# Optimization experiments

Measured on AMD Instinct MI355X. Metric: run time of the kernel, lower is better.

The kernel has to match this reference:

```python
import math
import jax, jax.numpy as jnp
import numpy as np

MODEL_DIM = 256
NUM_HEADS = 8
HEAD_DIM = MODEL_DIM // NUM_HEADS
B, S = 4, 2048


def setup_inputs() -> dict:
    key = jax.random.key(0)
    ks = jax.random.split(key, 9)
    d = MODEL_DIM
    lim = 1.0 / math.sqrt(d)  # torch nn.Linear init range
    def lin(k):
        k1, k2 = jax.random.split(k)
        W = jax.random.uniform(k1, (d, d), jnp.float32, -lim, lim)
        b = jax.random.uniform(k2, (d,), jnp.float32, -lim, lim)
        return W, b
    Wq, bq = lin(ks[0])
    Wk, bk = lin(ks[1])
    Wv, bv = lin(ks[2])
    Wo, bo = lin(ks[3])
    q = jax.random.normal(ks[4], (B, S, d), jnp.float32)
    q_mask = jnp.ones((B, S), dtype=bool)
    return {"q": q, "q_mask": q_mask, "Wq": Wq, "bq": bq, "Wk": Wk, "bk": bk,
            "Wv": Wv, "bv": bv, "Wo": Wo, "bo": bo}


def reference(q, q_mask, Wq, bq, Wk, bk, Wv, bv, Wo, bo):
    b, s, d = q.shape
    h, hd = NUM_HEADS, HEAD_DIM
    # merge_masks: kv_mask defaults to q_mask (self-attention), pad_mask -> float bias
    pad = q_mask[:, :, None] & q_mask[:, None, :]            # [b, s, s] recv x send
    bias = jnp.where(pad, 0.0, -jnp.inf).astype(q.dtype)      # additive attn bias
    # projections, split heads: [b, s, d] -> [b, h, s, hd]
    def proj(x, W, bb):
        return (x @ W.T + bb).reshape(b, s, h, hd).transpose(0, 2, 1, 3)
    qh = proj(q, Wq, bq)
    kh = proj(q, Wk, bk)
    vh = proj(q, Wv, bv)
    # NOTE: original scales by sqrt(model_dim), not sqrt(head_dim)
    qh = qh / math.sqrt(d)
    scores = jnp.einsum('bhqe,bhke->bhqk', qh, kh) + bias[:, None, :, :]
    attn = jax.nn.softmax(scores, axis=-1)
    out = jnp.einsum('bhqk,bhke->bhqe', attn, vh)             # [b, h, s, hd]
    out = out.transpose(0, 2, 1, 3).reshape(b, s, d)
    out = out @ Wo.T + bo
    return jnp.nan_to_num(out)
```

## Files before the change

### kernel.cpp

```cpp
#include <hip/hip_runtime.h>
#include <hip/hip_bf16.h>

typedef __attribute__((ext_vector_type(8))) short bf16x8;
typedef __attribute__((ext_vector_type(4))) short bf16x4;
typedef __attribute__((ext_vector_type(4))) float f32x4;
typedef unsigned short ushort_t;
typedef unsigned int uint_t;

__device__ __forceinline__ ushort_t f2bf(float f) {
  unsigned int u = __builtin_bit_cast(unsigned int, f);
  u += 0x7fffu + ((u >> 16) & 1u);
  return (ushort_t)(u >> 16);
}

__device__ __forceinline__ bf16x8 cvt8(f32x4 a, f32x4 b) {
  bf16x8 r;
  r[0] = (short)f2bf(a[0]); r[1] = (short)f2bf(a[1]);
  r[2] = (short)f2bf(a[2]); r[3] = (short)f2bf(a[3]);
  r[4] = (short)f2bf(b[0]); r[5] = (short)f2bf(b[1]);
  r[6] = (short)f2bf(b[2]); r[7] = (short)f2bf(b[3]);
  return r;
}

#if __has_builtin(__builtin_amdgcn_exp2f)
#define EXP2(x) __builtin_amdgcn_exp2f(x)
#else
#define EXP2(x) __expf(0.69314718056f * (x))
#endif

__device__ __forceinline__ f32x4 mfma16(bf16x4 a, bf16x4 b, f32x4 c) {
#if __has_builtin(__builtin_amdgcn_mfma_f32_16x16x16bf16_1k)
  return __builtin_amdgcn_mfma_f32_16x16x16bf16_1k(a, b, c, 0, 0, 0);
#else
  f32x4 d;
  asm volatile(
      "v_mfma_f32_16x16x16_bf16 %0, %1, %2, %3\n\ts_nop 7\n\ts_nop 7"
      : "=&v"(d)
      : "v"(a), "v"(b), "v"(c));
  return d;
#endif
}

__device__ __forceinline__ void gld_lds16(const void* g, void* l) {
  __builtin_amdgcn_global_load_lds(
      (const __attribute__((address_space(1))) unsigned int*)g,
      (__attribute__((address_space(3))) unsigned int*)l, 16, 0, 0);
}

__global__ __launch_bounds__(256) void prep2_kernel(
    const float* __restrict__ x, const float* __restrict__ Wq,
    const float* __restrict__ Wk, const float* __restrict__ Wv,
    const float* __restrict__ Wo, ushort_t* __restrict__ xb,
    ushort_t* __restrict__ Wb, ushort_t* __restrict__ Wob) {
  const int blk = blockIdx.x;
  const float* src;
  ushort_t* dst;
  int base;
  if (blk < 1024)      { src = x;  dst = xb;          base = blk * 2048; }
  else if (blk < 1056) { src = Wq; dst = Wb;          base = (blk - 1024) * 2048; }
  else if (blk < 1088) { src = Wk; dst = Wb + 65536;  base = (blk - 1056) * 2048; }
  else if (blk < 1120) { src = Wv; dst = Wb + 131072; base = (blk - 1088) * 2048; }
  else                 { src = Wo; dst = Wob;         base = (blk - 1120) * 2048; }
  const int i = base + threadIdx.x * 8;
  const f32x4 a = *(const f32x4*)(src + i);
  const f32x4 b = *(const f32x4*)(src + i + 4);
  *(bf16x8*)(dst + i) = cvt8(a, b);
}

__global__ __launch_bounds__(256) void qkv2_kernel(
    const ushort_t* __restrict__ xb, const ushort_t* __restrict__ Wb,
    const float* __restrict__ bq, const float* __restrict__ bk,
    const float* __restrict__ bv, ushort_t* __restrict__ qh,
    ushort_t* __restrict__ kh, ushort_t* __restrict__ vT) {
  __shared__ ushort_t Xs[2][2][2048], Ws[2][2][2048];
  const int tid = threadIdx.x;
  const int wid = tid >> 6, lane = tid & 63;
  const int l15 = lane & 15, lg = lane >> 4;
  const int row0 = blockIdx.x * 64;
  const int col0 = blockIdx.y * 64;
  const bool isV = (blockIdx.y >= 8);
  const char* XpB = (const char*)(xb + (size_t)row0 * 256);
  const char* WpB = (const char*)(Wb + (size_t)col0 * 256);
  const uint_t gsrc =
      (uint_t)((tid >> 2) * 512 + (((tid & 3) ^ ((tid >> 3) & 3)) << 4));
  const int kswz = (lg ^ ((l15 >> 1) & 3)) << 4;
  const int mrow = (wid >> 1) * 32, ncol = (wid & 1) * 32;
  f32x4 acc[2][2] = {};

#define STG(buf, t)                                                   \
  {                                                                   \
    gld_lds16(XpB + (t) * 64 + gsrc, (char*)Xs[buf][0] + wid * 1024); \
    gld_lds16(XpB + ((t) + 1) * 64 + gsrc,                            \
              (char*)Xs[buf][1] + wid * 1024);                        \
    gld_lds16(WpB + (t) * 64 + gsrc, (char*)Ws[buf][0] + wid * 1024); \
    gld_lds16(WpB + ((t) + 1) * 64 + gsrc,                            \
              (char*)Ws[buf][1] + wid * 1024);                        \
  }

#define CMP(XS, WS)                                                          \
  {                                                                          \
    const char* xs = (const char*)XS;                                        \
    const char* ws = (const char*)WS;                                        \
    bf16x8 af[2], bfr[2];                                                    \
    _Pragma("unroll") for (int m = 0; m < 2; ++m) af[m] =                    \
        *(const bf16x8*)(xs + (mrow + m * 16 + l15) * 64 + kswz);            \
    _Pragma("unroll") for (int n = 0; n < 2; ++n) bfr[n] =                   \
        *(const bf16x8*)(ws + (ncol + n * 16 + l15) * 64 + kswz);            \
    if (isV) {                                                               \
      _Pragma("unroll") for (int m = 0; m < 2; ++m) _Pragma("unroll")        \
          for (int n = 0; n < 2; ++n) acc[m][n] =                            \
              __builtin_amdgcn_mfma_f32_16x16x32_bf16(bfr[n], af[m],         \
                                                      acc[m][n], 0, 0, 0);   \
    } else {                                                                 \
      _Pragma("unroll") for (int m = 0; m < 2; ++m) _Pragma("unroll")        \
          for (int n = 0; n < 2; ++n) acc[m][n] =                            \
              __builtin_amdgcn_mfma_f32_16x16x32_bf16(af[m], bfr[n],         \
                                                      acc[m][n], 0, 0, 0);   \
    }                                                                        \
  }

  STG(0, 0)
  __syncthreads();
  for (int t = 0; t < 8; t += 4) {
    if (t + 2 < 8) STG(1, t + 2)
    CMP(Xs[0][0], Ws[0][0])
    CMP(Xs[0][1], Ws[0][1])
    __syncthreads();
    if (t + 4 < 8) STG(0, t + 4)
    CMP(Xs[1][0], Ws[1][0])
    CMP(Xs[1][1], Ws[1][1])
    __syncthreads();
  }
#undef STG
#undef CMP

  if (!isV) {
#pragma unroll
    for (int n = 0; n < 2; ++n) {
      const int gcol = col0 + ncol + n * 16 + l15;
      const bool isQ = (gcol < 256);
      const int c = gcol & 255;
      const float bias = (isQ ? bq : bk)[c];
      ushort_t* dst = isQ ? qh : kh;
      const float scale = isQ ? 0.0901684400f : 1.0f;
      const int h = c >> 5, e = c & 31;
#pragma unroll
      for (int m = 0; m < 2; ++m)
#pragma unroll
        for (int j = 0; j < 4; ++j) {
          const int grow = row0 + mrow + m * 16 + lg * 4 + j;
          const int b_ = grow >> 11, s_ = grow & 2047;
          dst[(size_t)((b_ * 8 + h) * 2048 + s_) * 32 + e] =
              f2bf((acc[m][n][j] + bias) * scale);
        }
    }
  } else {
#pragma unroll
    for (int n = 0; n < 2; ++n)
#pragma unroll
      for (int j = 0; j < 4; ++j) {
        const int c = col0 + ncol - 512 + n * 16 + lg * 4 + j;
        const float bias = bv[c];
        const int h = c >> 5, e = c & 31;
#pragma unroll
        for (int m = 0; m < 2; ++m) {
          const int grow = row0 + mrow + m * 16 + l15;
          const int b_ = grow >> 11, s_ = grow & 2047;
          vT[((size_t)(b_ * 8 + h) * 32 + e) * 2048 + s_] =
              f2bf(acc[m][n][j] + bias);
        }
      }
  }
}

__global__ __launch_bounds__(256) void oproj2_kernel(
    const ushort_t* __restrict__ a, const ushort_t* __restrict__ Wob,
    const float* __restrict__ bo, float* __restrict__ out) {
  __shared__ ushort_t Xs[2][2][2048], Ws[2][2][2048];
  const int tid = threadIdx.x;
  const int wid = tid >> 6, lane = tid & 63;
  const int l15 = lane & 15, lg = lane >> 4;
  const int row0 = blockIdx.x * 64;
  const int col0 = blockIdx.y * 64;
  const char* XpB = (const char*)(a + (size_t)row0 * 256);
  const char* WpB = (const char*)(Wob + (size_t)col0 * 256);
  const uint_t gsrc =
      (uint_t)((tid >> 2) * 512 + (((tid & 3) ^ ((tid >> 3) & 3)) << 4));
  const int kswz = (lg ^ ((l15 >> 1) & 3)) << 4;
  const int mrow = (wid >> 1) * 32, ncol = (wid & 1) * 32;
  f32x4 acc[2][2] = {};

#define STG(buf, t)                                                   \
  {                                                                   \
    gld_lds16(XpB + (t) * 64 + gsrc, (char*)Xs[buf][0] + wid * 1024); \
    gld_lds16(XpB + ((t) + 1) * 64 + gsrc,                            \
              (char*)Xs[buf][1] + wid * 1024);                        \
    gld_lds16(WpB + (t) * 64 + gsrc, (char*)Ws[buf][0] + wid * 1024); \
    gld_lds16(WpB + ((t) + 1) * 64 + gsrc,                            \
              (char*)Ws[buf][1] + wid * 1024);                        \
  }

#define CMP(XS, WS)                                                          \
  {                                                                          \
    const char* xs = (const char*)XS;                                        \
    const char* ws = (const char*)WS;                                        \
    bf16x8 af[2], bfr[2];                                                    \
    _Pragma("unroll") for (int m = 0; m < 2; ++m) af[m] =                    \
        *(const bf16x8*)(xs + (mrow + m * 16 + l15) * 64 + kswz);            \
    _Pragma("unroll") for (int n = 0; n < 2; ++n) bfr[n] =                   \
        *(const bf16x8*)(ws + (ncol + n * 16 + l15) * 64 + kswz);            \
    _Pragma("unroll") for (int m = 0; m < 2; ++m) _Pragma("unroll")          \
        for (int n = 0; n < 2; ++n) acc[m][n] =                              \
            __builtin_amdgcn_mfma_f32_16x16x32_bf16(af[m], bfr[n],           \
                                                    acc[m][n], 0, 0, 0);     \
  }

  STG(0, 0)
  __syncthreads();
  for (int t = 0; t < 8; t += 4) {
    if (t + 2 < 8) STG(1, t + 2)
    CMP(Xs[0][0], Ws[0][0])
    CMP(Xs[0][1], Ws[0][1])
    __syncthreads();
    if (t + 4 < 8) STG(0, t + 4)
    CMP(Xs[1][0], Ws[1][0])
    CMP(Xs[1][1], Ws[1][1])
    __syncthreads();
  }
#undef STG
#undef CMP

#pragma unroll
  for (int n = 0; n < 2; ++n) {
    const int gcol = col0 + ncol + n * 16 + l15;
    const float bias = bo[gcol];
#pragma unroll
    for (int m = 0; m < 2; ++m)
#pragma unroll
      for (int j = 0; j < 4; ++j) {
        const int grow = row0 + mrow + m * 16 + lg * 4 + j;
        out[(size_t)grow * 256 + gcol] = acc[m][n][j] + bias;
      }
  }
}

__global__ __launch_bounds__(256) void attn_kernel(
    const ushort_t* __restrict__ qh, const ushort_t* __restrict__ kh,
    const ushort_t* __restrict__ vT, ushort_t* __restrict__ ao) {
  __shared__ ushort_t Ksh[4][2048];
  __shared__ ushort_t Vsh[4][2048];
  const int tid = threadIdx.x;
  const int wid = tid >> 6, lane = tid & 63;
  const int l15 = lane & 15, lg = lane >> 4;
  const int bh = blockIdx.x & 31;
  const int qg = blockIdx.x >> 5;
  const int q0 = qg * 64 + wid * 16;
  const ushort_t* Qp = qh + ((size_t)bh * 2048 + q0) * 32;
  const char* KpB = (const char*)(kh + (size_t)bh * 2048 * 32);
  const char* VpB = (const char*)(vT + (size_t)bh * 32 * 2048);
  const bf16x8 qf = *(const bf16x8*)(Qp + l15 * 32 + lg * 8);
  const bf16x4 ones = {(short)0x3F80, (short)0x3F80, (short)0x3F80,
                       (short)0x3F80};
  f32x4 oacc[2] = {};
  f32x4 dacc = {0.f, 0.f, 0.f, 0.f};

  const uint_t ksrc =
      (uint_t)((tid >> 2) * 64 + (((tid & 3) ^ ((tid >> 3) & 3)) << 4));
  const uint_t vsrc = (uint_t)((tid >> 3) * 4096 +
                               (((tid & 7) ^ ((tid >> 3) & 7)) << 4));
  const int kswz = (lg ^ ((l15 >> 1) & 3)) << 4;
  const int vlo = (lg & 1) << 3;
  const int e7 = l15 & 7;

#define STAGE(slot, tile)                                              \
  {                                                                    \
    gld_lds16(KpB + (tile) * 4096 + ksrc, (char*)Ksh[slot] + wid * 1024); \
    gld_lds16(VpB + (tile) * 128 + vsrc, (char*)Vsh[slot] + wid * 1024);  \
  }

#define COMPUTE(K, V)                                                          \
  {                                                                            \
    const char* kb = (const char*)K;                                           \
    const char* vb = (const char*)V;                                           \
    _Pragma("unroll") for (int t4 = 0; t4 < 4; ++t4) {                         \
      const bf16x8 kf = *(const bf16x8*)(kb + (t4 * 16 + l15) * 64 + kswz);    \
      const f32x4 sf = __builtin_amdgcn_mfma_f32_16x16x32_bf16(                \
          kf, qf, (f32x4){0, 0, 0, 0}, 0, 0, 0);                               \
      bf16x4 pa;                                                               \
      {                                                                        \
        union { bf16x4 v4; __hip_bfloat162 h2[2]; } u;                         \
        u.h2[0] = __float22bfloat162_rn(make_float2(EXP2(sf[0]), EXP2(sf[1])));\
        u.h2[1] = __float22bfloat162_rn(make_float2(EXP2(sf[2]), EXP2(sf[3])));\
        pa = u.v4;                                                             \
      }                                                                        \
      dacc = mfma16(pa, ones, dacc);                                           \
      const int vchunk = (((t4 * 2 + (lg >> 1)) ^ e7) << 4) + vlo;             \
      const bf16x4 v0 = *(const bf16x4*)(vb + l15 * 128 + vchunk);             \
      const bf16x4 v1 = *(const bf16x4*)(vb + (16 + l15) * 128 + vchunk);      \
      oacc[0] = mfma16(pa, v0, oacc[0]);                                       \
      oacc[1] = mfma16(pa, v1, oacc[1]);                                       \
    }                                                                          \
  }

#define WAITB(lit)                                          \
  {                                                         \
    asm volatile("s_waitcnt vmcnt(" lit ")" ::: "memory");  \
    __builtin_amdgcn_s_barrier();                           \
    __builtin_amdgcn_sched_barrier(0);                      \
  }

  STAGE(0, 0)
  STAGE(1, 1)
  for (int t = 0; t < 30; ++t) {
    STAGE((t + 2) & 3, t + 2)
    WAITB("4")
    __builtin_amdgcn_s_setprio(1);
    COMPUTE(Ksh[t & 3], Vsh[t & 3])
    __builtin_amdgcn_s_setprio(0);
  }
  WAITB("2")
  __builtin_amdgcn_s_setprio(1);
  COMPUTE(Ksh[2], Vsh[2])
  __builtin_amdgcn_s_setprio(0);
  WAITB("0")
  __builtin_amdgcn_s_setprio(1);
  COMPUTE(Ksh[3], Vsh[3])
  __builtin_amdgcn_s_setprio(0);
#undef STAGE
#undef COMPUTE
#undef WAITB

  const int b_ = bh >> 3, h = bh & 7;
#pragma unroll
  for (int j = 0; j < 4; ++j) {
    const float rd = 1.0f / dacc[j];
    const int s_ = q0 + 4 * lg + j;
#pragma unroll
    for (int et = 0; et < 2; ++et) {
      const int col = h * 32 + et * 16 + l15;
      ao[((size_t)(b_ * 2048) + s_) * 256 + col] = f2bf(oacc[et][j] * rd);
    }
  }
}

extern "C" void kernel_launch(void* const* d_in, const int* in_sizes, int n_in,
                              void* d_out, int out_size, void* d_ws,
                              size_t ws_size, hipStream_t stream) {
  const float* q = (const float*)d_in[0];
  const float* Wq = (const float*)d_in[2];
  const float* bq = (const float*)d_in[3];
  const float* Wk = (const float*)d_in[4];
  const float* bk = (const float*)d_in[5];
  const float* Wv = (const float*)d_in[6];
  const float* bv = (const float*)d_in[7];
  const float* Wo = (const float*)d_in[8];
  const float* bo = (const float*)d_in[9];

  ushort_t* qh = (ushort_t*)d_ws;
  ushort_t* kh = qh + (size_t)2097152;
  ushort_t* vT = kh + (size_t)2097152;
  ushort_t* xb_ao = vT + (size_t)2097152;
  ushort_t* Wb = xb_ao + (size_t)2097152;
  ushort_t* Wob = Wb + (size_t)196608;
  float* out = (float*)d_out;

  prep2_kernel<<<dim3(1152), 256, 0, stream>>>(q, Wq, Wk, Wv, Wo, xb_ao, Wb,
                                               Wob);
  qkv2_kernel<<<dim3(128, 12), 256, 0, stream>>>(xb_ao, Wb, bq, bk, bv, qh,
                                                 kh, vT);
  attn_kernel<<<dim3(1024), 256, 0, stream>>>(qh, kh, vT, xb_ao);
  oproj2_kernel<<<dim3(128, 4), 256, 0, stream>>>(xb_ao, Wob, bo, out);
}
```

Before: 62.17 us.

## Split attention KV range across two blocks and combine partial sums

Each attention block now handles half of the key/value sequence, which doubles the grid to 2048 blocks. The kernel writes unnormalized partial outputs and denominators into the output buffer used as scratch, and a new combine kernel adds the two halves and normalizes them. The LDS pipeline is cut to double buffering with an occupancy hint of 8 blocks per CU, aiming for more parallelism and latency hiding. The cost is an extra kernel launch, extra global traffic for the partials, and a bf16 rounding of the partial outputs before they are combined. Skipping the max subtraction is only safe because the scores need no max shift, which is already the case in the prior code.

```diff
diff --git a/kernel.cpp b/kernel.cpp
--- a/kernel.cpp
+++ b/kernel.cpp
@@ -11,6 +11,10 @@
   unsigned int u = __builtin_bit_cast(unsigned int, f);
   u += 0x7fffu + ((u >> 16) & 1u);
   return (ushort_t)(u >> 16);
+}
+
+__device__ __forceinline__ float bf2f(ushort_t u) {
+  return __builtin_bit_cast(float, ((uint_t)u) << 16);
 }
 
 __device__ __forceinline__ bf16x8 cvt8(f32x4 a, f32x4 b) {
@@ -244,20 +248,24 @@
   }
 }
 
-__global__ __launch_bounds__(256) void attn_kernel(
+__global__ __launch_bounds__(256, 8) void attn_kernel(
     const ushort_t* __restrict__ qh, const ushort_t* __restrict__ kh,
-    const ushort_t* __restrict__ vT, ushort_t* __restrict__ ao) {
-  __shared__ ushort_t Ksh[4][2048];
-  __shared__ ushort_t Vsh[4][2048];
+    const ushort_t* __restrict__ vT, ushort_t* __restrict__ O0,
+    ushort_t* __restrict__ O1, float* __restrict__ dpt) {
+  __shared__ ushort_t Ksh[2][2048];
+  __shared__ ushort_t Vsh[2][2048];
   const int tid = threadIdx.x;
   const int wid = tid >> 6, lane = tid & 63;
   const int l15 = lane & 15, lg = lane >> 4;
   const int bh = blockIdx.x & 31;
-  const int qg = blockIdx.x >> 5;
+  const int qg = (blockIdx.x >> 5) & 31;
+  const int half = blockIdx.x >> 10;
   const int q0 = qg * 64 + wid * 16;
   const ushort_t* Qp = qh + ((size_t)bh * 2048 + q0) * 32;
-  const char* KpB = (const char*)(kh + (size_t)bh * 2048 * 32);
-  const char* VpB = (const char*)(vT + (size_t)bh * 32 * 2048);
+  const char* KpH =
+      (const char*)(kh + (size_t)bh * 2048 * 32) + half * 65536;
+  const char* VpH =
+      (const char*)(vT + (size_t)bh * 32 * 2048) + half * 2048;
   const bf16x8 qf = *(const bf16x8*)(Qp + l15 * 32 + lg * 8);
   const bf16x4 ones = {(short)0x3F80, (short)0x3F80, (short)0x3F80,
                        (short)0x3F80};
@@ -272,10 +280,10 @@
   const int vlo = (lg & 1) << 3;
   const int e7 = l15 & 7;
 
-#define STAGE(slot, tile)                                              \
-  {                                                                    \
-    gld_lds16(KpB + (tile) * 4096 + ksrc, (char*)Ksh[slot] + wid * 1024); \
-    gld_lds16(VpB + (tile) * 128 + vsrc, (char*)Vsh[slot] + wid * 1024);  \
+#define STAGE(slot, tile)                                                  \
+  {                                                                        \
+    gld_lds16(KpH + (tile) * 4096 + ksrc, (char*)Ksh[slot] + wid * 1024);  \
+    gld_lds16(VpH + (tile) * 128 + vsrc, (char*)Vsh[slot] + wid * 1024);   \
   }
 
 #define COMPUTE(K, V)                                                          \
@@ -310,37 +318,59 @@
   }
 
   STAGE(0, 0)
-  STAGE(1, 1)
-  for (int t = 0; t < 30; ++t) {
-    STAGE((t + 2) & 3, t + 2)
-    WAITB("4")
+  for (int t = 0; t < 15; ++t) {
+    STAGE((t + 1) & 1, t + 1)
+    WAITB("2")
     __builtin_amdgcn_s_setprio(1);
-    COMPUTE(Ksh[t & 3], Vsh[t & 3])
+    COMPUTE(Ksh[t & 1], Vsh[t & 1])
     __builtin_amdgcn_s_setprio(0);
-  }
-  WAITB("2")
-  __builtin_amdgcn_s_setprio(1);
-  COMPUTE(Ksh[2], Vsh[2])
-  __builtin_amdgcn_s_setprio(0);
+    __builtin_amdgcn_s_barrier();
+  }
   WAITB("0")
   __builtin_amdgcn_s_setprio(1);
-  COMPUTE(Ksh[3], Vsh[3])
+  COMPUTE(Ksh[1], Vsh[1])
   __builtin_amdgcn_s_setprio(0);
 #undef STAGE
 #undef COMPUTE
 #undef WAITB
 
+  ushort_t* Op = half ? O1 : O0;
+  float* Dp = dpt + half * 65536;
   const int b_ = bh >> 3, h = bh & 7;
 #pragma unroll
   for (int j = 0; j < 4; ++j) {
-    const float rd = 1.0f / dacc[j];
     const int s_ = q0 + 4 * lg + j;
 #pragma unroll
     for (int et = 0; et < 2; ++et) {
       const int col = h * 32 + et * 16 + l15;
-      ao[((size_t)(b_ * 2048) + s_) * 256 + col] = f2bf(oacc[et][j] * rd);
+      Op[((size_t)(b_ * 2048) + s_) * 256 + col] = f2bf(oacc[et][j]);
     }
   }
+  if (l15 == 0) {
+#pragma unroll
+    for (int j = 0; j < 4; ++j)
+      Dp[(b_ * 8 + h) * 2048 + q0 + 4 * lg + j] = dacc[j];
+  }
+}
+
+__global__ __launch_bounds__(256) void combine_kernel(
+    ushort_t* __restrict__ O0, const ushort_t* __restrict__ O1,
+    const float* __restrict__ dpt) {
+  const int i8 = (blockIdx.x * 256 + threadIdx.x) * 8;
+  const int b = i8 >> 19;
+  const int s = (i8 >> 8) & 2047;
+  const int head = (i8 & 255) >> 5;
+  const int didx = (b * 8 + head) * 2048 + s;
+  const float rd = 1.0f / (dpt[didx] + dpt[65536 + didx]);
+  const bf16x8 a = *(const bf16x8*)(O0 + i8);
+  const bf16x8 c = *(const bf16x8*)(O1 + i8);
+  bf16x8 r;
+#pragma unroll
+  for (int k = 0; k < 8; ++k) {
+    const float f = bf2f((ushort_t)a[k]) + bf2f((ushort_t)c[k]);
+    r[k] = (short)f2bf(f * rd);
+  }
+  *(bf16x8*)(O0 + i8) = r;
 }
 
 extern "C" void kernel_launch(void* const* d_in, const int* in_sizes, int n_in,
@@ -363,11 +393,14 @@
   ushort_t* Wb = xb_ao + (size_t)2097152;
   ushort_t* Wob = Wb + (size_t)196608;
   float* out = (float*)d_out;
+  ushort_t* O1 = (ushort_t*)d_out;
+  float* dpt = (float*)d_out + 1048576;
 
   prep2_kernel<<<dim3(1152), 256, 0, stream>>>(q, Wq, Wk, Wv, Wo, xb_ao, Wb,
                                                Wob);
   qkv2_kernel<<<dim3(128, 12), 256, 0, stream>>>(xb_ao, Wb, bq, bk, bv, qh,
                                                  kh, vT);
-  attn_kernel<<<dim3(1024), 256, 0, stream>>>(qh, kh, vT, xb_ao);
+  attn_kernel<<<dim3(2048), 256, 0, stream>>>(qh, kh, vT, xb_ao, O1, dpt);
+  combine_kernel<<<dim3(1024), 256, 0, stream>>>(xb_ao, O1, dpt);
   oproj2_kernel<<<dim3(128, 4), 256, 0, stream>>>(xb_ao, Wob, bo, out);
 }
```

New measurement: 60.77 us. 2.3% less time.
